# Optimization experiments

Measured on AMD Instinct MI355X. Metric: run time of the kernel, lower is better.

The kernel has to match this reference:

```python
import jax, jax.numpy as jnp
import numpy as np

EPS = 1e-5

def _conv(x, w, pad):
    return jax.lax.conv_general_dilated(
        x, w, window_strides=(1, 1), padding=[(pad, pad), (pad, pad)],
        dimension_numbers=('NCHW', 'OIHW', 'NCHW'))

def _bn_relu(y, gamma, beta, mean, var):
    inv = gamma / jnp.sqrt(var + EPS)
    return jax.nn.relu(y * inv[None, :, None, None] + (beta - mean * inv)[None, :, None, None])

def setup_inputs() -> dict:
    key = jax.random.key(0)
    ks = jax.random.split(key, 20)
    B, L, D, H = 32, 144, 96, 64
    inp = {
        'x': jax.random.normal(ks[0], (B, L, H, H), dtype=jnp.float32),
        'w1': jax.random.normal(ks[1], (D, L, 3, 3), dtype=jnp.float32) * (1.0 / np.sqrt(L * 9)),
        'b1': jax.random.normal(ks[2], (D,), dtype=jnp.float32) * 0.01,
        'g1': jnp.ones((D,), jnp.float32), 'be1': jnp.zeros((D,), jnp.float32),
        'm1': jax.random.normal(ks[3], (D,), dtype=jnp.float32) * 0.1,
        'v1': jax.random.uniform(ks[4], (D,), jnp.float32, 0.5, 1.5),
        'w2': jax.random.normal(ks[5], (D, L, 5, 5), dtype=jnp.float32) * (1.0 / np.sqrt(L * 25)),
        'b2': jax.random.normal(ks[6], (D,), dtype=jnp.float32) * 0.01,
        'g2': jnp.ones((D,), jnp.float32), 'be2': jnp.zeros((D,), jnp.float32),
        'm2': jax.random.normal(ks[7], (D,), dtype=jnp.float32) * 0.1,
        'v2': jax.random.uniform(ks[8], (D,), jnp.float32, 0.5, 1.5),
        'w3': jax.random.normal(ks[9], (D, L, 7, 7), dtype=jnp.float32) * (1.0 / np.sqrt(L * 49)),
        'b3': jax.random.normal(ks[10], (D,), dtype=jnp.float32) * 0.01,
        'g3': jnp.ones((D,), jnp.float32), 'be3': jnp.zeros((D,), jnp.float32),
        'm3': jax.random.normal(ks[11], (D,), dtype=jnp.float32) * 0.1,
        'v3': jax.random.uniform(ks[12], (D,), jnp.float32, 0.5, 1.5),
        'wf': jax.random.normal(ks[13], (1, 3, 3, 3), dtype=jnp.float32) * (1.0 / np.sqrt(27)),
    }
    return inp

def reference(x, w1, b1, g1, be1, m1, v1, w2, b2, g2, be2, m2, v2, w3, b3, g3, be3, m3, v3, wf):
    # three multi-scale branches: conv + BN(eval) + ReLU
    x1 = _bn_relu(_conv(x, w1, 1) + b1[None, :, None, None], g1, be1, m1, v1)
    x2 = _bn_relu(_conv(x, w2, 2) + b2[None, :, None, None], g2, be2, m2, v2)
    x3 = _bn_relu(_conv(x, w3, 3) + b3[None, :, None, None], g3, be3, m3, v3)
    # per-channel fusion (num1=num2=num3=1): add / mean / max over the 3 branch slices
    add = x1 + x2 + x3
    avg = add * (1.0 / 3.0)
    mx = jnp.maximum(jnp.maximum(x1, x2), x3)
    B, D, H, W = add.shape
    # [B, D, 3, H, W] -> fold D into batch, apply shared 3->1 conv per channel
    s = jnp.stack([add, avg, mx], axis=2).reshape(B * D, 3, H, W)
    out = _conv(s, wf, 1).reshape(B, D, H, W)
    return out
```

## Files before the change

### kernel.cpp

```cpp
#include <hip/hip_runtime.h>
#include <hip/hip_bf16.h>

typedef __hip_bfloat16 bf16;
typedef short v8s __attribute__((ext_vector_type(8)));
typedef float f32x4 __attribute__((ext_vector_type(4)));
typedef unsigned int u32x4 __attribute__((ext_vector_type(4)));

#define B_  32
#define L_  144
#define D_  96
#define HW_ 64

#define PIXSTRIDE 80
#define WPACK_ELEMS (83*5*96*32)
#define ABUF_HALF 18432

__device__ __forceinline__ unsigned short f2bf(float f) {
    union { float f; unsigned int u; } x{f};
    unsigned int r = x.u + 0x7fffu + ((x.u >> 16) & 1u);
    return (unsigned short)(r >> 16);
}
__device__ __forceinline__ float bf2f(unsigned short u) {
    union { unsigned int u; float f; } x{(unsigned int)u << 16};
    return x.f;
}

__global__ __launch_bounds__(256) void prep_weights(
    const float* __restrict__ w1, const float* __restrict__ w2,
    const float* __restrict__ w3, unsigned short* __restrict__ wpack)
{
    int i = blockIdx.x * 256 + threadIdx.x;
    if (i >= WPACK_ELEMS) return;
    const int lt = i & 31;
    const int d  = (i >> 5) % 96;
    const int r  = (i >> 5) / 96;
    const int q  = r % 5;
    const int T  = r / 5;
    const int l  = q * 32 + lt;
    float v = 0.f;
    if (l < L_) {
        if (T < 49)      v = w3[(d * L_ + l) * 49 + T];
        else if (T < 74) v = w2[(d * L_ + l) * 25 + (T - 49)];
        else             v = w1[(d * L_ + l) * 9  + (T - 74)];
    }
    wpack[i] = f2bf(v);
}

template<int KSZ, int TBASE, int MODE>
__global__ __launch_bounds__(512, 4) void conv_branch(
    const float* __restrict__ x, const unsigned short* __restrict__ wpack,
    const float* __restrict__ bb, const float* __restrict__ gg,
    const float* __restrict__ bbe, const float* __restrict__ mm,
    const float* __restrict__ vv,
    float* __restrict__ outp)
{
    constexpr int PAD  = KSZ / 2;
    constexpr int PXR  = 16 + 2 * PAD;
    constexpr int NPIX = PXR * PXR;
    constexpr int NT   = KSZ * KSZ;
    constexpr int NG   = (NT + 2) / 3;

    __shared__ __align__(16) unsigned char patchB[NPIX * PIXSTRIDE];
    __shared__ __align__(16) unsigned char AbufRaw[2 * ABUF_HALF];
    __shared__ float bns[96 * 2];

    const int t    = threadIdx.x;
    const int lane = t & 63;
    const int wid  = t >> 6;
    const int dhalf = wid >> 2;
    const int ptb   = (wid & 3) * 4;
    const int lo = lane & 15;
    const int hi = lane >> 4;

    const int st = blockIdx.x;
    const int h0 = (st >> 2) << 4;
    const int w0 = (st & 3) << 4;
    const int b  = blockIdx.y;

    const int laneBoff = lo * PIXSTRIDE + hi * 16;

    const bool pvalid = (t < NPIX);
    const int pr = t / PXR, pc = t - pr * PXR;
    const int gh = h0 - PAD + pr, gw = w0 - PAD + pc;
    const bool inb = pvalid && ((unsigned)gh < 64u) && ((unsigned)gw < 64u);
    const float* xb = x + (((size_t)b * L_) << 12);
    const long goff = (long)(gh << 6) + gw;

    if (t < 96) {
        const float iv = gg[t] * rsqrtf(vv[t] + 1e-5f);
        bns[t*2+0] = iv;
        bns[t*2+1] = fmaf(bb[t] - mm[t], iv, bbe[t]);
    }

    f32x4 acc[3][4];
    #pragma unroll
    for (int dt = 0; dt < 3; ++dt)
        #pragma unroll
        for (int pp = 0; pp < 4; ++pp) acc[dt][pp] = (f32x4)0.f;

    const int laneAsrc = (lane & 15) * 32 + (lane >> 4) * 8;

    for (int q = 0; q < 5; ++q) {
        if (pvalid) {
            if (q * 32 + 31 < L_) {
                #pragma unroll
                for (int l0 = 0; l0 < 32; l0 += 8) {
                    const long gbase = (long)(q * 32 + l0) * 4096 + goff;
                    const float f0 = inb ? xb[gbase]           : 0.f;
                    const float f1 = inb ? xb[gbase + 4096]    : 0.f;
                    const float f2 = inb ? xb[gbase + 2*4096]  : 0.f;
                    const float f3 = inb ? xb[gbase + 3*4096]  : 0.f;
                    const float f4 = inb ? xb[gbase + 4*4096]  : 0.f;
                    const float f5 = inb ? xb[gbase + 5*4096]  : 0.f;
                    const float f6 = inb ? xb[gbase + 6*4096]  : 0.f;
                    const float f7 = inb ? xb[gbase + 7*4096]  : 0.f;
                    const unsigned int a0 = (unsigned int)f2bf(f0) | ((unsigned int)f2bf(f1) << 16);
                    const unsigned int a1 = (unsigned int)f2bf(f2) | ((unsigned int)f2bf(f3) << 16);
                    const unsigned int a2 = (unsigned int)f2bf(f4) | ((unsigned int)f2bf(f5) << 16);
                    const unsigned int a3 = (unsigned int)f2bf(f6) | ((unsigned int)f2bf(f7) << 16);
                    const u32x4 v = {a0, a1, a2, a3};
                    *(u32x4*)(patchB + t * PIXSTRIDE + l0 * 2) = v;
                }
            } else {
                #pragma unroll
                for (int l0 = 0; l0 < 32; l0 += 8) {
                    const int lg = q * 32 + l0;
                    const long gbase = (long)lg * 4096 + goff;
                    const float f0 = (inb && lg + 0 < L_) ? xb[gbase]          : 0.f;
                    const float f1 = (inb && lg + 1 < L_) ? xb[gbase + 4096]   : 0.f;
                    const float f2 = (inb && lg + 2 < L_) ? xb[gbase + 2*4096] : 0.f;
                    const float f3 = (inb && lg + 3 < L_) ? xb[gbase + 3*4096] : 0.f;
                    const float f4 = (inb && lg + 4 < L_) ? xb[gbase + 4*4096] : 0.f;
                    const float f5 = (inb && lg + 5 < L_) ? xb[gbase + 5*4096] : 0.f;
                    const float f6 = (inb && lg + 6 < L_) ? xb[gbase + 6*4096] : 0.f;
                    const float f7 = (inb && lg + 7 < L_) ? xb[gbase + 7*4096] : 0.f;
                    const unsigned int a0 = (unsigned int)f2bf(f0) | ((unsigned int)f2bf(f1) << 16);
                    const unsigned int a1 = (unsigned int)f2bf(f2) | ((unsigned int)f2bf(f3) << 16);
                    const unsigned int a2 = (unsigned int)f2bf(f4) | ((unsigned int)f2bf(f5) << 16);
                    const unsigned int a3 = (unsigned int)f2bf(f6) | ((unsigned int)f2bf(f7) << 16);
                    const u32x4 v = {a0, a1, a2, a3};
                    *(u32x4*)(patchB + t * PIXSTRIDE + l0 * 2) = v;
                }
            }
        }

        auto stageA = [&](int tapLo, int bufOff) {
            const int rem  = NT - tapLo;
            const int nch  = (rem < 3 ? rem : 3) * 6;
            const unsigned short* gq = wpack
                + (size_t)(TBASE + tapLo) * 15360 + (size_t)q * 3072 + laneAsrc;
            for (int c = wid; c < nch; c += 8) {
                const int tapIdx = c / 6;
                const int r = c - tapIdx * 6;
                const unsigned short* g = gq + (size_t)tapIdx * 15360 + r * 512;
                __builtin_amdgcn_global_load_lds(
                    (const __attribute__((address_space(1))) unsigned int*)g,
                    (__attribute__((address_space(3))) unsigned int*)(AbufRaw + bufOff + c * 1024),
                    16, 0, 0);
            }
        };

        stageA(0, 0);
        __syncthreads();

        for (int tg = 0; tg < NG; ++tg) {
            if (tg + 1 < NG) stageA((tg + 1) * 3, ((tg + 1) & 1) * ABUF_HALF);

            const unsigned char* Ab = AbufRaw + (tg & 1) * ABUF_HALF;
            const int tapLo = tg * 3;
            const int rem = NT - tapLo;
            const int ntap = rem < 3 ? rem : 3;
            #pragma unroll 1
            for (int ti = 0; ti < ntap; ++ti) {
                const int tt = tapLo + ti;
                const int kh = tt / KSZ, kw = tt - kh * KSZ;
                const unsigned char* Abase = Ab + (ti * 6 + dhalf * 3) * 1024 + lane * 16;
                const v8s A0 = *(const v8s*)(Abase);
                const v8s A1 = *(const v8s*)(Abase + 1024);
                const v8s A2 = *(const v8s*)(Abase + 2048);
                const int rb0 = (ptb + kh) * PXR;
                v8s Bv[4];
                #pragma unroll
                for (int pp = 0; pp < 4; ++pp)
                    Bv[pp] = *(const v8s*)(patchB + (rb0 + pp * PXR + kw) * PIXSTRIDE + laneBoff);
                #pragma unroll
                for (int pp = 0; pp < 4; ++pp) {
                    acc[0][pp] = __builtin_amdgcn_mfma_f32_16x16x32_bf16(A0, Bv[pp], acc[0][pp], 0, 0, 0);
                    acc[1][pp] = __builtin_amdgcn_mfma_f32_16x16x32_bf16(A1, Bv[pp], acc[1][pp], 0, 0, 0);
                    acc[2][pp] = __builtin_amdgcn_mfma_f32_16x16x32_bf16(A2, Bv[pp], acc[2][pp], 0, 0, 0);
                }
            }
            __syncthreads();
        }
    }

    #pragma unroll
    for (int dt = 0; dt < 3; ++dt) {
        #pragma unroll
        for (int reg = 0; reg < 4; ++reg) {
            const int d = dhalf * 48 + dt * 16 + hi * 4 + reg;
            const float iv = bns[d*2+0], cv = bns[d*2+1];
            unsigned short* pl = (unsigned short*)(outp + (((size_t)b * D_ + d) << 12));
            #pragma unroll
            for (int pp = 0; pp < 4; ++pp) {
                const float y = fmaxf(0.f, fmaf(acc[dt][pp][reg], iv, cv));
                const int idx = ((h0 + ptb + pp) << 6) + w0 + lo;
                if constexpr (MODE == 0) {
                    pl[4096 + idx] = f2bf(y);
                } else if constexpr (MODE == 1) {
                    pl[idx] = f2bf(y);
                } else {
                    const float y2 = bf2f(pl[idx]);
                    const float y3 = bf2f(pl[4096 + idx]);
                    const float av = y + y2 + y3;
                    const float mv = fmaxf(y, fmaxf(y2, y3));
                    pl[idx]        = f2bf(av);
                    pl[4096 + idx] = f2bf(mv);
                }
            }
        }
    }
}

__global__ __launch_bounds__(256) void fuse_kernel(
    const float* __restrict__ wf, float* __restrict__ out)
{
    const int p = blockIdx.x;
    const int t = threadIdx.x;
    __shared__ float sa[66 * 66];
    __shared__ float sm[66 * 66];
    const bf16* base = (const bf16*)(out + ((size_t)p << 12));

    for (int i = t; i < 66 * 66; i += 256) {
        const int c = i % 66, r = i / 66;
        const int gh = r - 1, gw = c - 1;
        float va = 0.f, vm = 0.f;
        if (gh >= 0 && gh < 64 && gw >= 0 && gw < 64) {
            va = __bfloat162float(base[(gh << 6) + gw]);
            vm = __bfloat162float(base[4096 + (gh << 6) + gw]);
        }
        sa[i] = va; sm[i] = vm;
    }

    float wa[9], wm[9];
    #pragma unroll
    for (int j = 0; j < 9; ++j) {
        wa[j] = wf[j] + wf[9 + j] * (1.f / 3.f);
        wm[j] = wf[18 + j];
    }
    __syncthreads();

    float* op = out + ((size_t)p << 12);
    for (int i = t; i < 4096; i += 256) {
        const int h = i >> 6, w = i & 63;
        float acc = 0.f;
        #pragma unroll
        for (int kh = 0; kh < 3; ++kh) {
            #pragma unroll
            for (int kw = 0; kw < 3; ++kw) {
                acc = fmaf(sa[(h + kh) * 66 + (w + kw)], wa[kh * 3 + kw], acc);
                acc = fmaf(sm[(h + kh) * 66 + (w + kw)], wm[kh * 3 + kw], acc);
            }
        }
        op[i] = acc;
    }
}

extern "C" void kernel_launch(void* const* d_in, const int* in_sizes, int n_in,
                              void* d_out, int out_size, void* d_ws, size_t ws_size,
                              hipStream_t stream)
{
    const float* x   = (const float*)d_in[0];
    const float* w1  = (const float*)d_in[1];
    const float* b1  = (const float*)d_in[2];
    const float* g1  = (const float*)d_in[3];
    const float* be1 = (const float*)d_in[4];
    const float* m1  = (const float*)d_in[5];
    const float* v1  = (const float*)d_in[6];
    const float* w2  = (const float*)d_in[7];
    const float* b2  = (const float*)d_in[8];
    const float* g2  = (const float*)d_in[9];
    const float* be2 = (const float*)d_in[10];
    const float* m2  = (const float*)d_in[11];
    const float* v2  = (const float*)d_in[12];
    const float* w3  = (const float*)d_in[13];
    const float* b3  = (const float*)d_in[14];
    const float* g3  = (const float*)d_in[15];
    const float* be3 = (const float*)d_in[16];
    const float* m3  = (const float*)d_in[17];
    const float* v3  = (const float*)d_in[18];
    const float* wf  = (const float*)d_in[19];
    float* out = (float*)d_out;

    unsigned short* wpack = (unsigned short*)d_ws;

    prep_weights<<<(WPACK_ELEMS + 255) / 256, 256, 0, stream>>>(w1, w2, w3, wpack);

    dim3 gridA(16, B_);
    conv_branch<7, 0, 0><<<gridA, 512, 0, stream>>>(x, wpack, b3, g3, be3, m3, v3, out);
    conv_branch<5, 49, 1><<<gridA, 512, 0, stream>>>(x, wpack, b2, g2, be2, m2, v2, out);
    conv_branch<3, 74, 2><<<gridA, 512, 0, stream>>>(x, wpack, b1, g1, be1, m1, v1, out);

    fuse_kernel<<<B_ * D_, 256, 0, stream>>>(wf, out);
}
```

Measured before the change: 397.5 us.

## Reorder conv taps column-major to reuse B fragments across kernel rows

Weights are repacked in column-major tap order (kw outer, kh inner), and the tap loop now walks each kernel column in groups of up to three rows. Each group loads a sliding window of NTAP+3 patch rows once and reuses them across taps and pixel rows, instead of reloading four B fragments per tap. This is meant to cut LDS reads per MFMA. In exchange there are more tap groups, and therefore more barriers and A-staging rounds (e.g. 7x3 groups instead of 17 for the 7x7 kernel), plus more registers held for the B window.

```diff
diff --git a/kernel.cpp b/kernel.cpp
--- a/kernel.cpp
+++ b/kernel.cpp
@@ -39,9 +39,9 @@
     const int l  = q * 32 + lt;
     float v = 0.f;
     if (l < L_) {
-        if (T < 49)      v = w3[(d * L_ + l) * 49 + T];
-        else if (T < 74) v = w2[(d * L_ + l) * 25 + (T - 49)];
-        else             v = w1[(d * L_ + l) * 9  + (T - 74)];
+        if (T < 49)      { const int U = T;      v = w3[(d * L_ + l) * 49 + (U % 7) * 7 + U / 7]; }
+        else if (T < 74) { const int U = T - 49; v = w2[(d * L_ + l) * 25 + (U % 5) * 5 + U / 5]; }
+        else             { const int U = T - 74; v = w1[(d * L_ + l) * 9  + (U % 3) * 3 + U / 3]; }
     }
     wpack[i] = f2bf(v);
 }
@@ -57,8 +57,8 @@
     constexpr int PAD  = KSZ / 2;
     constexpr int PXR  = 16 + 2 * PAD;
     constexpr int NPIX = PXR * PXR;
-    constexpr int NT   = KSZ * KSZ;
-    constexpr int NG   = (NT + 2) / 3;
+    constexpr int NGc  = (KSZ + 2) / 3;
+    constexpr int NG   = KSZ * NGc;
 
     __shared__ __align__(16) unsigned char patchB[NPIX * PIXSTRIDE];
     __shared__ __align__(16) unsigned char AbufRaw[2 * ABUF_HALF];
@@ -144,9 +144,8 @@
             }
         }
 
-        auto stageA = [&](int tapLo, int bufOff) {
-            const int rem  = NT - tapLo;
-            const int nch  = (rem < 3 ? rem : 3) * 6;
+        auto stageA = [&](int tapLo, int ntapP, int bufOff) {
+            const int nch = ntapP * 6;
             const unsigned short* gq = wpack
                 + (size_t)(TBASE + tapLo) * 15360 + (size_t)q * 3072 + laneAsrc;
             for (int c = wid; c < nch; c += 8) {
@@ -160,38 +159,49 @@
             }
         };
 
-        stageA(0, 0);
+        stageA(0, 3, 0);
         __syncthreads();
 
-        for (int tg = 0; tg < NG; ++tg) {
-            if (tg + 1 < NG) stageA((tg + 1) * 3, ((tg + 1) & 1) * ABUF_HALF);
-
-            const unsigned char* Ab = AbufRaw + (tg & 1) * ABUF_HALF;
-            const int tapLo = tg * 3;
-            const int rem = NT - tapLo;
-            const int ntap = rem < 3 ? rem : 3;
-            #pragma unroll 1
-            for (int ti = 0; ti < ntap; ++ti) {
-                const int tt = tapLo + ti;
-                const int kh = tt / KSZ, kw = tt - kh * KSZ;
-                const unsigned char* Abase = Ab + (ti * 6 + dhalf * 3) * 1024 + lane * 16;
-                const v8s A0 = *(const v8s*)(Abase);
-                const v8s A1 = *(const v8s*)(Abase + 1024);
-                const v8s A2 = *(const v8s*)(Abase + 2048);
-                const int rb0 = (ptb + kh) * PXR;
-                v8s Bv[4];
-                #pragma unroll
-                for (int pp = 0; pp < 4; ++pp)
-                    Bv[pp] = *(const v8s*)(patchB + (rb0 + pp * PXR + kw) * PIXSTRIDE + laneBoff);
-                #pragma unroll
-                for (int pp = 0; pp < 4; ++pp) {
-                    acc[0][pp] = __builtin_amdgcn_mfma_f32_16x16x32_bf16(A0, Bv[pp], acc[0][pp], 0, 0, 0);
-                    acc[1][pp] = __builtin_amdgcn_mfma_f32_16x16x32_bf16(A1, Bv[pp], acc[1][pp], 0, 0, 0);
-                    acc[2][pp] = __builtin_amdgcn_mfma_f32_16x16x32_bf16(A2, Bv[pp], acc[2][pp], 0, 0, 0);
-                }
-            }
-            __syncthreads();
-        }
+#define PROCESS_GROUP(GIDX, NTAP)                                              \
+        {                                                                      \
+            const int g_ = col * NGc + (GIDX);                                 \
+            const int gn_ = g_ + 1;                                            \
+            if (gn_ < NG) {                                                    \
+                const int coln_ = gn_ / NGc;                                   \
+                const int gidxn_ = gn_ - coln_ * NGc;                          \
+                const int rem_ = KSZ - gidxn_ * 3;                             \
+                stageA(coln_ * KSZ + gidxn_ * 3,                               \
+                       rem_ < 3 ? rem_ : 3, (gn_ & 1) * ABUF_HALF);            \
+            }                                                                  \
+            const unsigned char* Ab = AbufRaw + (g_ & 1) * ABUF_HALF;          \
+            const int pixBase = (ptb + (GIDX) * 3) * PXR + col;                \
+            v8s Bw[(NTAP) + 3];                                                \
+            _Pragma("unroll")                                                  \
+            for (int j = 0; j < (NTAP) + 3; ++j)                               \
+                Bw[j] = *(const v8s*)(patchB + (pixBase + j * PXR) * PIXSTRIDE + laneBoff); \
+            _Pragma("unroll")                                                  \
+            for (int ti = 0; ti < (NTAP); ++ti) {                              \
+                const unsigned char* Abase = Ab + (ti * 6 + dhalf * 3) * 1024 + lane * 16; \
+                const v8s A0 = *(const v8s*)(Abase);                           \
+                const v8s A1 = *(const v8s*)(Abase + 1024);                    \
+                const v8s A2 = *(const v8s*)(Abase + 2048);                    \
+                _Pragma("unroll")                                              \
+                for (int pp = 0; pp < 4; ++pp) {                               \
+                    acc[0][pp] = __builtin_amdgcn_mfma_f32_16x16x32_bf16(A0, Bw[ti + pp], acc[0][pp], 0, 0, 0); \
+                    acc[1][pp] = __builtin_amdgcn_mfma_f32_16x16x32_bf16(A1, Bw[ti + pp], acc[1][pp], 0, 0, 0); \
+                    acc[2][pp] = __builtin_amdgcn_mfma_f32_16x16x32_bf16(A2, Bw[ti + pp], acc[2][pp], 0, 0, 0); \
+                }                                                              \
+            }                                                                  \
+            __syncthreads();                                                   \
+        }
+
+        #pragma unroll 1
+        for (int col = 0; col < KSZ; ++col) {
+            PROCESS_GROUP(0, 3)
+            if constexpr (KSZ == 5) { PROCESS_GROUP(1, 2) }
+            if constexpr (KSZ == 7) { PROCESS_GROUP(1, 3) PROCESS_GROUP(2, 1) }
+        }
+#undef PROCESS_GROUP
     }
 
     #pragma unroll
```

After: 380.9 us. -4.2%, faster.
